# Optimization experiments

Measured on AMD Instinct MI355X. Metric: run time of the kernel, lower is better.

Reference implementation:

```python
import jax, jax.numpy as jnp
import numpy as np

B, C, H, W = 4, 512, 64, 64
C8 = C // 8


def setup_inputs() -> dict:
    key = jax.random.key(0)
    ks = jax.random.split(key, 12)
    s = lambda fan_in: 1.0 / np.sqrt(fan_in)
    return {
        "final_encoded": jax.random.normal(ks[0], (B, C, H, W), jnp.float32),
        "total": jax.random.normal(ks[1], (B, C, H, W), jnp.float32),
        # 1x1 conv weights (out, in) and biases
        "Wq": jax.random.normal(ks[2], (C8, C), jnp.float32) * s(C),
        "bq": jax.random.normal(ks[3], (C8,), jnp.float32) * s(C),
        "Wk": jax.random.normal(ks[4], (C8, C), jnp.float32) * s(C),
        "bk": jax.random.normal(ks[5], (C8,), jnp.float32) * s(C),
        "Wv": jax.random.normal(ks[6], (C, C), jnp.float32) * s(C),
        "bv": jax.random.normal(ks[7], (C,), jnp.float32) * s(C),
        # learned additive positional tensors
        "height_tensor": jax.random.normal(ks[8], (1, C8, H, 1), jnp.float32),
        "width_tensor": jax.random.normal(ks[9], (1, C8, 1, W), jnp.float32),
        "gamma": jnp.zeros((1,), jnp.float32),
    }


def reference(final_encoded, total, Wq, bq, Wk, bk, Wv, bv, height_tensor, width_tensor, gamma):
    b, c, h, w = final_encoded.shape
    c8 = c // 8
    hw = h * w
    # 1x1 convs as channel matmuls
    q = jnp.einsum("oc,bchw->bohw", Wq, total) + bq[None, :, None, None]
    k = jnp.einsum("oc,bchw->bohw", Wk, final_encoded) + bk[None, :, None, None]
    v = jnp.einsum("oc,bchw->bohw", Wv, final_encoded) + bv[None, :, None, None]
    pq = q.reshape(b, c8, hw).transpose(0, 2, 1)   # [B, HW, C8]
    pk = k.reshape(b, c8, hw)                      # [B, C8, HW]
    pv = v.reshape(b, c, hw)                       # [B, C, HW]
    energy = jnp.einsum("bnc,bcm->bnm", pq, pk)    # [B, HW, HW] content energy
    pos = (height_tensor + width_tensor).reshape(c8, hw)  # [C8, HW] additive positional bias basis
    energy = energy + jnp.einsum("bnc,cm->bnm", pq, pos)
    attention = jax.nn.softmax(energy, axis=-1)
    # out = bmm(value, attention^T)
    out = jnp.einsum("bcm,bnm->bcn", pv, attention).reshape(b, c, h, w)
    return gamma * out + final_encoded
```

## Files before the change

kernel.cpp:

```cpp
#include <hip/hip_runtime.h>
#include <hip/hip_bf16.h>

#define B_   4
#define C_   512
#define C8_  64
#define HW_  4096

typedef short bf16x8 __attribute__((ext_vector_type(8)));
typedef float f32x4  __attribute__((ext_vector_type(4)));

__device__ __forceinline__ unsigned short f2bf(float f) {
  union { unsigned int i; float f; } x; x.f = f;
  unsigned int r = x.i + 0x7fffu + ((x.i >> 16) & 1u);
  return (unsigned short)(r >> 16);
}

__device__ __forceinline__ unsigned int cvtpk(float lo, float hi) {
  unsigned int r;
  asm("v_cvt_pk_bf16_f32 %0, %1, %2" : "=v"(r) : "v"(lo), "v"(hi));
  return r;
}

__device__ __forceinline__ float fexp2(float x) {
  float r;
  asm("v_exp_f32 %0, %1" : "=v"(r) : "v"(x));
  return r;
}

#define MFMA(a, b, c) __builtin_amdgcn_mfma_f32_16x16x32_bf16((a), (b), (c), 0, 0, 0)

#define LOG2E 1.44269504f
#define NEG20LOG2E -28.8539008f


__global__ __launch_bounds__(640) void proj_kernel(
    const float* __restrict__ total, const float* __restrict__ fe,
    const float* __restrict__ Wq, const float* __restrict__ bq,
    const float* __restrict__ Wk, const float* __restrict__ bk,
    const float* __restrict__ Wv, const float* __restrict__ bv,
    const float* __restrict__ ht, const float* __restrict__ wt,
    unsigned short* __restrict__ Qh, unsigned short* __restrict__ Kh,
    unsigned short* __restrict__ Vn) {
  __shared__ __align__(16) unsigned short Ws[640 * 72];
  __shared__ __align__(16) unsigned short Xf[64 * 72];
  __shared__ __align__(16) unsigned short Xt[64 * 72];

  const int t = threadIdx.x;
  const int b = blockIdx.y;
  const int x = blockIdx.x;
  const int m0 = x * 64;
  const int lane = t & 63, w = t >> 6, ln = lane & 15, quad = lane >> 4;

  const int c4 = t & 15;
  const int orow = t >> 4;

  f32x4 acc[4][4];
#pragma unroll
  for (int ct = 0; ct < 4; ++ct)
#pragma unroll
    for (int mt = 0; mt < 4; ++mt) acc[ct][mt] = f32x4{0.f, 0.f, 0.f, 0.f};

  for (int kb = 0; kb < 8; ++kb) {
    const int c0 = kb * 64;
#pragma unroll
    for (int i = 0; i < 16; ++i) {
      const int o = i * 40 + orow;
      const float* src = (o < 64) ? &Wq[(size_t)o * C_]
                       : (o < 128) ? &Wk[(size_t)(o - 64) * C_]
                                   : &Wv[(size_t)(o - 128) * C_];
      f32x4 wv = *(const f32x4*)&src[c0 + c4 * 4];
      *(uint2*)&Ws[o * 72 + c4 * 4] =
          make_uint2(cvtpk(wv[0], wv[1]), cvtpk(wv[2], wv[3]));
    }
    if (t < 512) {
      const int t2 = t & 255;
      const float* Xsrc = (t < 256) ? fe : total;
      unsigned short* Xdst = (t < 256) ? Xf : Xt;
      const int rc4 = t2 >> 4, mq = t2 & 15;
      f32x4 xv[4];
#pragma unroll
      for (int k = 0; k < 4; ++k)
        xv[k] = *(const f32x4*)&Xsrc[((size_t)b * C_ + c0 + rc4 * 4 + k) * HW_ + m0 + mq * 4];
#pragma unroll
      for (int j = 0; j < 4; ++j)
        *(uint2*)&Xdst[(mq * 4 + j) * 72 + rc4 * 4] =
            make_uint2(cvtpk(xv[0][j], xv[1][j]), cvtpk(xv[2][j], xv[3][j]));
    }
    __syncthreads();
    const unsigned short* Xsel = (w == 0) ? Xt : Xf;
    bf16x8 aw[4][2], bx[4][2];
#pragma unroll
    for (int ct = 0; ct < 4; ++ct) {
      aw[ct][0] = *(const bf16x8*)&Ws[(w * 64 + ct * 16 + ln) * 72 + quad * 8];
      aw[ct][1] = *(const bf16x8*)&Ws[(w * 64 + ct * 16 + ln) * 72 + 32 + quad * 8];
    }
#pragma unroll
    for (int mt = 0; mt < 4; ++mt) {
      bx[mt][0] = *(const bf16x8*)&Xsel[(mt * 16 + ln) * 72 + quad * 8];
      bx[mt][1] = *(const bf16x8*)&Xsel[(mt * 16 + ln) * 72 + 32 + quad * 8];
    }
#pragma unroll
    for (int ct = 0; ct < 4; ++ct)
#pragma unroll
      for (int mt = 0; mt < 4; ++mt) {
        acc[ct][mt] = MFMA(aw[ct][0], bx[mt][0], acc[ct][mt]);
        acc[ct][mt] = MFMA(aw[ct][1], bx[mt][1], acc[ct][mt]);
      }
    __syncthreads();
  }

  if (w == 0) {
#pragma unroll
    for (int ct = 0; ct < 4; ++ct)
#pragma unroll
      for (int mt = 0; mt < 4; ++mt)
#pragma unroll
        for (int r = 0; r < 4; ++r) {
          const int o = ct * 16 + quad * 4 + r;
          const float val = (acc[ct][mt][r] + bq[o]) * LOG2E;
          const size_t idx = ((size_t)b * 512 + (x * 4 + mt) * 2 + (ct >> 1)) * 512
                           + ((((ct & 1) << 1) | (quad >> 1))) * 128
                           + ln * 8 + ((quad & 1) << 2) + r;
          Qh[idx] = f2bf(val);
        }
  } else if (w == 1) {
#pragma unroll
    for (int ct = 0; ct < 4; ++ct)
#pragma unroll
      for (int mt = 0; mt < 4; ++mt)
#pragma unroll
        for (int r = 0; r < 4; ++r) {
          const int o = ct * 16 + quad * 4 + r;
          const float val = acc[ct][mt][r] + bk[o] + ht[o * 64 + x] + wt[o * 64 + mt * 16 + ln];
          const size_t idx = ((size_t)b * 512 + (x * 4 + mt) * 2 + (ct >> 1)) * 512
                           + ((((ct & 1) << 1) | (quad >> 1))) * 128
                           + ln * 8 + ((quad & 1) << 2) + r;
          Kh[idx] = f2bf(val);
        }
  } else {
#pragma unroll
    for (int ct = 0; ct < 4; ++ct) {
      const int cht = w * 4 - 8 + ct;
#pragma unroll
      for (int r = 0; r < 4; ++r) {
        const float bz = bv[cht * 16 + quad * 4 + r];
#pragma unroll
        for (int mt = 0; mt < 4; ++mt) {
          const size_t idx = (((size_t)b * 32 + cht) * 128 + (size_t)x * 2 + (mt >> 1)) * 512
                           + (((mt & 1) * 2) + (ln >> 3)) * 128 + (quad * 4 + r) * 8 + (ln & 7);
          Vn[idx] = f2bf(acc[ct][mt][r] + bz);
        }
      }
    }
  }
}

__global__ __launch_bounds__(512, 2) void flash_kernel(
    const unsigned short* __restrict__ Qh, const unsigned short* __restrict__ Kh,
    const unsigned short* __restrict__ Vn, const float* __restrict__ fe,
    const float* __restrict__ gamma, float* __restrict__ out) {
  __shared__ __align__(16) unsigned short Ps[2][128 * 64];
  __shared__ float Red[2][128];

  const int t = threadIdx.x;
  const int n = blockIdx.x;
  const int xcd = n & 7;
  const int b = xcd & 3;
  const int ch0 = (xcd >> 2) * 256;
  const int q0 = (n >> 3) * 128;
  const int lane = t & 63, w = t >> 6, ln = lane & 15, quad = lane >> 4;
  const int qs = w & 3;
  const int kh = w >> 2;
  const int swz = (ln & 7) << 4;

  const unsigned short* Qb = Qh + (size_t)b * 512 * 512;
  const unsigned short* Kb = Kh + (size_t)b * 512 * 512;
  const unsigned short* Vbase = Vn + ((size_t)b * 32 + (ch0 >> 4)) * (128 * 512);

  bf16x8 aq[2][2];
#pragma unroll
  for (int sub = 0; sub < 2; ++sub)
#pragma unroll
    for (int hf = 0; hf < 2; ++hf)
      aq[sub][hf] = *(const bf16x8*)
          &Qb[((size_t)((q0 >> 4) + qs * 2 + sub) * 2 + hf) * 512 + lane * 8];

  const f32x4 CINIT = {NEG20LOG2E, NEG20LOG2E, NEG20LOG2E, NEG20LOG2E};

  float Sacc0 = 0.f, Sacc1 = 0.f;
  f32x4 acc[2][8];
#pragma unroll
  for (int mt = 0; mt < 2; ++mt)
#pragma unroll
    for (int nt = 0; nt < 8; ++nt) acc[mt][nt] = f32x4{0.f, 0.f, 0.f, 0.f};

  bf16x8 kf[2][2];
  bf16x8 vf[2][2];

  auto loadK = [&](int it) {
#pragma unroll
    for (int nt = 0; nt < 2; ++nt)
#pragma unroll
      for (int hf = 0; hf < 2; ++hf)
        kf[nt][hf] = *(const bf16x8*)&Kb[((size_t)(it * 4 + kh * 2 + nt) * 2 + hf) * 512 + lane * 8];
  };
  auto loadV = [&](int it) {
#pragma unroll
    for (int mt = 0; mt < 2; ++mt)
#pragma unroll
      for (int kc = 0; kc < 2; ++kc)
        vf[mt][kc] = *(const bf16x8*)&Vbase[(((size_t)(w * 2 + mt)) * 128 + it * 2 + kc) * 512 + lane * 8];
  };

  const int qr0 = qs * 32 + ln;

  auto qkWrite = [&](char* Pw) {
    f32x4 e00 = MFMA(kf[0][0], aq[0][0], CINIT);
    e00 = MFMA(kf[0][1], aq[0][1], e00);
    f32x4 e01 = MFMA(kf[1][0], aq[0][0], CINIT);
    e01 = MFMA(kf[1][1], aq[0][1], e01);
    f32x4 e10 = MFMA(kf[0][0], aq[1][0], CINIT);
    e10 = MFMA(kf[0][1], aq[1][1], e10);
    f32x4 e11 = MFMA(kf[1][0], aq[1][0], CINIT);
    e11 = MFMA(kf[1][1], aq[1][1], e11);
#pragma unroll
    for (int kn = 0; kn < 2; ++kn) {
      const f32x4 ea = (kn == 0) ? e00 : e01;
      const float a0 = fexp2(ea[0]), a1 = fexp2(ea[1]);
      const float a2 = fexp2(ea[2]), a3 = fexp2(ea[3]);
      Sacc0 += (a0 + a1) + (a2 + a3);
      *(uint2*)(Pw + ((qr0 * 128 + kh * 64 + kn * 32 + quad * 8) ^ swz)) =
          make_uint2(cvtpk(a0, a1), cvtpk(a2, a3));
      const f32x4 eb = (kn == 0) ? e10 : e11;
      const float b0 = fexp2(eb[0]), b1 = fexp2(eb[1]);
      const float b2 = fexp2(eb[2]), b3 = fexp2(eb[3]);
      Sacc1 += (b0 + b1) + (b2 + b3);
      *(uint2*)(Pw + (((qr0 + 16) * 128 + kh * 64 + kn * 32 + quad * 8) ^ swz)) =
          make_uint2(cvtpk(b0, b1), cvtpk(b2, b3));
    }
  };

  loadK(0);
  loadV(0);

  qkWrite((char*)Ps[0]);
  loadK(1);
  asm volatile("s_waitcnt lgkmcnt(0)" ::: "memory");
  __builtin_amdgcn_s_barrier();
  asm volatile("" ::: "memory");

  for (int it = 0; it < 64; ++it) {
    char* Prd = (char*)Ps[it & 1];
    char* Pwr = (char*)Ps[(it + 1) & 1];
    bf16x8 bp[8];
#pragma unroll
    for (int nt = 0; nt < 8; ++nt)
      bp[nt] = *(const bf16x8*)(Prd + ((((nt * 16 + ln) * 128 + quad * 16)) ^ swz));
    if (it < 63) {
      __builtin_amdgcn_s_setprio(1);
      qkWrite(Pwr);
      __builtin_amdgcn_s_setprio(0);
      if (it < 62) loadK(it + 2);
    }
    __builtin_amdgcn_s_setprio(1);
#pragma unroll
    for (int mt = 0; mt < 2; ++mt)
#pragma unroll
      for (int nt = 0; nt < 8; ++nt)
        acc[mt][nt] = MFMA(vf[mt][0], bp[nt], acc[mt][nt]);
    __builtin_amdgcn_s_setprio(0);
#pragma unroll
    for (int nt = 0; nt < 8; ++nt)
      bp[nt] = *(const bf16x8*)(Prd + ((((nt * 16 + ln) * 128 + 64 + quad * 16)) ^ swz));
    __builtin_amdgcn_s_setprio(1);
#pragma unroll
    for (int mt = 0; mt < 2; ++mt)
#pragma unroll
      for (int nt = 0; nt < 8; ++nt)
        acc[mt][nt] = MFMA(vf[mt][1], bp[nt], acc[mt][nt]);
    __builtin_amdgcn_s_setprio(0);
    if (it < 63) {
      loadV(it + 1);
      asm volatile("s_waitcnt lgkmcnt(0)" ::: "memory");
      __builtin_amdgcn_s_barrier();
      asm volatile("" ::: "memory");
    }
  }

  {
    float s = Sacc0;
    s += __shfl_xor(s, 16);
    s += __shfl_xor(s, 32);
    if (quad == 0) Red[kh][qr0] = s;
    float s1 = Sacc1;
    s1 += __shfl_xor(s1, 16);
    s1 += __shfl_xor(s1, 32);
    if (quad == 0) Red[kh][qr0 + 16] = s1;
  }
  __syncthreads();
  float rsv[8];
#pragma unroll
  for (int nt = 0; nt < 8; ++nt)
    rsv[nt] = 1.0f / (Red[0][nt * 16 + ln] + Red[1][nt * 16 + ln]);

  const float g = gamma[0];
#pragma unroll
  for (int mt = 0; mt < 2; ++mt) {
#pragma unroll
    for (int r = 0; r < 4; ++r) {
      const int ch = ch0 + w * 32 + mt * 16 + quad * 4 + r;
      const size_t base = ((size_t)b * C_ + ch) * HW_ + q0;
#pragma unroll
      for (int nt = 0; nt < 8; ++nt) {
        const size_t idx = base + nt * 16 + ln;
        out[idx] = g * (acc[mt][nt][r] * rsv[nt]) + fe[idx];
      }
    }
  }
}

extern "C" void kernel_launch(void* const* d_in, const int* in_sizes, int n_in,
                              void* d_out, int out_size, void* d_ws, size_t ws_size,
                              hipStream_t stream) {
  const float* fe    = (const float*)d_in[0];
  const float* total = (const float*)d_in[1];
  const float* Wq    = (const float*)d_in[2];
  const float* bq    = (const float*)d_in[3];
  const float* Wk    = (const float*)d_in[4];
  const float* bk    = (const float*)d_in[5];
  const float* Wv    = (const float*)d_in[6];
  const float* bv    = (const float*)d_in[7];
  const float* ht    = (const float*)d_in[8];
  const float* wt    = (const float*)d_in[9];
  const float* gamma = (const float*)d_in[10];
  float* out = (float*)d_out;

  unsigned short* Qh = (unsigned short*)d_ws;
  unsigned short* Kh = Qh + (size_t)B_ * HW_ * C8_;
  unsigned short* Vn = Kh + (size_t)B_ * HW_ * C8_;

  proj_kernel<<<dim3(64, B_), 640, 0, stream>>>(total, fe, Wq, bq, Wk, bk,
                                                Wv, bv, ht, wt, Qh, Kh, Vn);
  flash_kernel<<<dim3(256), 512, 0, stream>>>(Qh, Kh, Vn, fe, gamma, out);
}
```

Baseline: 221.7 us.

## Split flash kernel channel range across twice as many blocks

Each flash block now covers 128 value channels instead of 256, so the grid doubles to 512 blocks and each wave holds half the accumulator tiles and V fragments. Launch bounds are raised to 4 blocks per CU to use the lower register footprint for occupancy. The cost is that every block recomputes the QK^T scores and softmax exponentials for its query tile, so that work is now done four times per query tile instead of twice, and more blocks contend for the P shared buffers.

```diff
diff --git a/kernel.cpp b/kernel.cpp
--- a/kernel.cpp
+++ b/kernel.cpp
@@ -155,7 +155,7 @@
   }
 }
 
-__global__ __launch_bounds__(512, 2) void flash_kernel(
+__global__ __launch_bounds__(512, 4) void flash_kernel(
     const unsigned short* __restrict__ Qh, const unsigned short* __restrict__ Kh,
     const unsigned short* __restrict__ Vn, const float* __restrict__ fe,
     const float* __restrict__ gamma, float* __restrict__ out) {
@@ -164,10 +164,10 @@
 
   const int t = threadIdx.x;
   const int n = blockIdx.x;
-  const int xcd = n & 7;
-  const int b = xcd & 3;
-  const int ch0 = (xcd >> 2) * 256;
-  const int q0 = (n >> 3) * 128;
+  const int g = n & 15;
+  const int b = g & 3;
+  const int ch0 = (g >> 2) * 128;
+  const int q0 = (n >> 4) * 128;
   const int lane = t & 63, w = t >> 6, ln = lane & 15, quad = lane >> 4;
   const int qs = w & 3;
   const int kh = w >> 2;
@@ -188,14 +188,12 @@
   const f32x4 CINIT = {NEG20LOG2E, NEG20LOG2E, NEG20LOG2E, NEG20LOG2E};
 
   float Sacc0 = 0.f, Sacc1 = 0.f;
-  f32x4 acc[2][8];
-#pragma unroll
-  for (int mt = 0; mt < 2; ++mt)
-#pragma unroll
-    for (int nt = 0; nt < 8; ++nt) acc[mt][nt] = f32x4{0.f, 0.f, 0.f, 0.f};
+  f32x4 acc[8];
+#pragma unroll
+  for (int nt = 0; nt < 8; ++nt) acc[nt] = f32x4{0.f, 0.f, 0.f, 0.f};
 
   bf16x8 kf[2][2];
-  bf16x8 vf[2][2];
+  bf16x8 vf[2];
 
   auto loadK = [&](int it) {
 #pragma unroll
@@ -206,10 +204,8 @@
   };
   auto loadV = [&](int it) {
 #pragma unroll
-    for (int mt = 0; mt < 2; ++mt)
-#pragma unroll
-      for (int kc = 0; kc < 2; ++kc)
-        vf[mt][kc] = *(const bf16x8*)&Vbase[(((size_t)(w * 2 + mt)) * 128 + it * 2 + kc) * 512 + lane * 8];
+    for (int kc = 0; kc < 2; ++kc)
+      vf[kc] = *(const bf16x8*)&Vbase[((size_t)w * 128 + it * 2 + kc) * 512 + lane * 8];
   };
 
   const int qr0 = qs * 32 + ln;
@@ -264,20 +260,16 @@
     }
     __builtin_amdgcn_s_setprio(1);
 #pragma unroll
-    for (int mt = 0; mt < 2; ++mt)
-#pragma unroll
-      for (int nt = 0; nt < 8; ++nt)
-        acc[mt][nt] = MFMA(vf[mt][0], bp[nt], acc[mt][nt]);
+    for (int nt = 0; nt < 8; ++nt)
+      acc[nt] = MFMA(vf[0], bp[nt], acc[nt]);
     __builtin_amdgcn_s_setprio(0);
 #pragma unroll
     for (int nt = 0; nt < 8; ++nt)
       bp[nt] = *(const bf16x8*)(Prd + ((((nt * 16 + ln) * 128 + 64 + quad * 16)) ^ swz));
     __builtin_amdgcn_s_setprio(1);
 #pragma unroll
-    for (int mt = 0; mt < 2; ++mt)
-#pragma unroll
-      for (int nt = 0; nt < 8; ++nt)
-        acc[mt][nt] = MFMA(vf[mt][1], bp[nt], acc[mt][nt]);
+    for (int nt = 0; nt < 8; ++nt)
+      acc[nt] = MFMA(vf[1], bp[nt], acc[nt]);
     __builtin_amdgcn_s_setprio(0);
     if (it < 63) {
       loadV(it + 1);
@@ -303,18 +295,15 @@
   for (int nt = 0; nt < 8; ++nt)
     rsv[nt] = 1.0f / (Red[0][nt * 16 + ln] + Red[1][nt * 16 + ln]);
 
-  const float g = gamma[0];
-#pragma unroll
-  for (int mt = 0; mt < 2; ++mt) {
-#pragma unroll
-    for (int r = 0; r < 4; ++r) {
-      const int ch = ch0 + w * 32 + mt * 16 + quad * 4 + r;
-      const size_t base = ((size_t)b * C_ + ch) * HW_ + q0;
-#pragma unroll
-      for (int nt = 0; nt < 8; ++nt) {
-        const size_t idx = base + nt * 16 + ln;
-        out[idx] = g * (acc[mt][nt][r] * rsv[nt]) + fe[idx];
-      }
+  const float g_ = gamma[0];
+#pragma unroll
+  for (int r = 0; r < 4; ++r) {
+    const int ch = ch0 + w * 16 + quad * 4 + r;
+    const size_t base = ((size_t)b * C_ + ch) * HW_ + q0;
+#pragma unroll
+    for (int nt = 0; nt < 8; ++nt) {
+      const size_t idx = base + nt * 16 + ln;
+      out[idx] = g_ * (acc[nt][r] * rsv[nt]) + fe[idx];
     }
   }
 }
@@ -341,5 +330,5 @@
 
   proj_kernel<<<dim3(64, B_), 640, 0, stream>>>(total, fe, Wq, bq, Wk, bk,
                                                 Wv, bv, ht, wt, Qh, Kh, Vn);
-  flash_kernel<<<dim3(256), 512, 0, stream>>>(Qh, Kh, Vn, fe, gamma, out);
-}
+  flash_kernel<<<dim3(512), 512, 0, stream>>>(Qh, Kh, Vn, fe, gamma, out);
+}
```

Result: slower. 291.4 us (+31.4%).
